# Performance work log

Hardware: AMD Instinct MI355X
Metric: run time of the kernel (lower is better)

Reference implementation:

```python
import jax, jax.numpy as jnp
import numpy as np

BN_EPS = 1e-5


def _bn(y, g, b, m, v):
    # BatchNorm1d in eval mode (running stats), faithful to torch's affine BN
    return (y - m) * jax.lax.rsqrt(v + BN_EPS) * g + b


def setup_inputs() -> dict:
    key = jax.random.key(0)
    ks = jax.random.split(key, 6)
    N, E, C_IN, C_OUT = 20000, 640000, 128, 256
    x = jax.random.normal(ks[0], (N, C_IN), dtype=jnp.float32)
    tpl_edge_index = jax.random.randint(ks[1], (2, E), 0, N, dtype=jnp.int64)
    def lin(k, o, i):
        return jax.random.normal(k, (o, i), dtype=jnp.float32) * 0.05
    inp = {
        'x': x,
        'tpl_edge_index': tpl_edge_index,
        'W1': lin(ks[2], C_OUT, 2 * C_IN), 'b1': jnp.zeros((C_OUT,), jnp.float32),
        'g1': jnp.ones((C_OUT,), jnp.float32), 'be1': jnp.zeros((C_OUT,), jnp.float32),
        'm1': jnp.zeros((C_OUT,), jnp.float32), 'v1': jnp.ones((C_OUT,), jnp.float32),
        'W2': lin(ks[3], C_OUT, C_OUT), 'b2': jnp.zeros((C_OUT,), jnp.float32),
        'g2': jnp.ones((C_OUT,), jnp.float32), 'be2': jnp.zeros((C_OUT,), jnp.float32),
        'm2': jnp.zeros((C_OUT,), jnp.float32), 'v2': jnp.ones((C_OUT,), jnp.float32),
        'W3': lin(ks[4], C_OUT, C_OUT), 'b3': jnp.zeros((C_OUT,), jnp.float32),
        'g3': jnp.ones((C_OUT,), jnp.float32), 'be3': jnp.zeros((C_OUT,), jnp.float32),
        'm3': jnp.zeros((C_OUT,), jnp.float32), 'v3': jnp.ones((C_OUT,), jnp.float32),
    }
    return inp


def reference(x, tpl_edge_index, W1, b1, g1, be1, m1, v1,
              W2, b2, g2, be2, m2, v2, W3, b3, g3, be3, m3, v3):
    N = x.shape[0]
    # remove_self_loops + add_self_loops: under max aggregation, duplicate
    # self-loop messages (x_j - x_i == 0) are idempotent, so appending one
    # self-loop per node is mathematically identical.
    loops = jnp.arange(N, dtype=tpl_edge_index.dtype)
    src = jnp.concatenate([tpl_edge_index[0], loops])  # x_j indices
    tgt = jnp.concatenate([tpl_edge_index[1], loops])  # x_i / aggregation indices
    x_i = x[tgt]                                       # [E+N, C_in]
    x_j = x[src]
    h = jnp.concatenate([x_i, x_j - x_i], axis=1)      # [E+N, 2*C_in]
    h = _bn(jax.nn.relu(h @ W1.T + b1), g1, be1, m1, v1)
    h = _bn(jax.nn.relu(h @ W2.T + b2), g2, be2, m2, v2)
    agg = jax.ops.segment_max(h, tgt, num_segments=N)  # scatter-max -> [N, C_out]
    out = _bn(jax.nn.relu(agg @ W3.T + b3), g3, be3, m3, v3)
    return out
```

## Files before the change

kernel.cpp:

```cpp
#include <hip/hip_runtime.h>
#include <stdint.h>

#define BN_EPS 1e-5f

typedef __bf16 bf16x8 __attribute__((ext_vector_type(8)));
typedef float  f32x4  __attribute__((ext_vector_type(4)));

__device__ __forceinline__ unsigned short f2bf(float f) {
    unsigned u = __float_as_uint(f);
    unsigned r = (u + 0x7FFFu + ((u >> 16) & 1u)) >> 16;
    return (unsigned short)r;
}
__device__ __forceinline__ unsigned pk2(float a, float b) {
    return (unsigned)f2bf(a) | ((unsigned)f2bf(b) << 16);
}
__device__ __forceinline__ unsigned ar2(unsigned p, unsigned q) {
    float pl = __uint_as_float(p << 16), ql = __uint_as_float(q << 16);
    float ph = __uint_as_float(p & 0xFFFF0000u), qh = __uint_as_float(q & 0xFFFF0000u);
    return pk2(fmaxf(pl + ql, 0.f), fmaxf(ph + qh, 0.f));
}
__device__ __forceinline__ unsigned short bfkey(unsigned short h) {
    return (h & 0x8000u) ? (unsigned short)(~h) : (unsigned short)(h | 0x8000u);
}
__device__ __forceinline__ unsigned short unbfkey(unsigned short k) {
    return (k & 0x8000u) ? (unsigned short)(k & 0x7FFFu) : (unsigned short)(~k);
}
__device__ __forceinline__ unsigned unb2(unsigned k0, unsigned k1) {
    return (unsigned)unbfkey((unsigned short)k0)
         | ((unsigned)unbfkey((unsigned short)k1) << 16);
}
__device__ __forceinline__ unsigned kk2(float a, float b) {
    return (unsigned)bfkey(f2bf(a)) | ((unsigned)bfkey(f2bf(b)) << 16);
}
__device__ __forceinline__ int swz(int row, int k) {
    const int blk = k >> 3;
    const int sb = (blk & 24) | ((blk ^ row) & 7);
    return (row << 8) + (sb << 3) + (k & 7);
}
__device__ __forceinline__ int swz128(int row, int k) {
    const int blk = k >> 3;
    const int sb = (blk & 8) | ((blk ^ row) & 7);
    return (row << 7) + (sb << 3) + (k & 7);
}

__global__ void prep_kernel(
    const float* __restrict__ x, const int* __restrict__ eidx,
    int E, int M, int NX,
    const float* __restrict__ W1, const float* __restrict__ W2, const float* __restrict__ W3,
    const float* __restrict__ b1, const float* __restrict__ g1, const float* __restrict__ be1,
    const float* __restrict__ m1, const float* __restrict__ v1,
    const float* __restrict__ b2, const float* __restrict__ g2, const float* __restrict__ be2,
    const float* __restrict__ m2, const float* __restrict__ v2,
    const float* __restrict__ b3, const float* __restrict__ g3, const float* __restrict__ be3,
    const float* __restrict__ m3, const float* __restrict__ v3,
    unsigned short* __restrict__ W1b, unsigned short* __restrict__ W2b,
    unsigned short* __restrict__ W3b, float* __restrict__ consts,
    unsigned short* __restrict__ xb, unsigned* __restrict__ count)
{
    const int idx = blockIdx.x * 256 + threadIdx.x;
    if (idx < 65536) {
        const int row = idx >> 8, c = idx & 255;
        float w1v = (c < 128) ? (W1[row * 256 + c] - W1[row * 256 + c + 128])
                              : W1[row * 256 + c];
        W1b[idx] = f2bf(w1v);
        const float s1c = g1[c] * rsqrtf(v1[c] + BN_EPS);
        W2b[idx] = f2bf(W2[idx] * s1c);
        W3b[idx] = f2bf(W3[idx]);
    }
    if (idx < 768) {
        const int l = idx >> 8, c = idx & 255;
        const float* bp  = l == 0 ? b1  : (l == 1 ? b2  : b3);
        const float* gp  = l == 0 ? g1  : (l == 1 ? g2  : g3);
        const float* bep = l == 0 ? be1 : (l == 1 ? be2 : be3);
        const float* mp  = l == 0 ? m1  : (l == 1 ? m2  : m3);
        const float* vp  = l == 0 ? v1  : (l == 1 ? v2  : v3);
        const float s = gp[c] * rsqrtf(vp[c] + BN_EPS);
        float bias = bp[c];
        if (l == 1) {
            float acc = 0.f;
            for (int k = 0; k < 256; k++) {
                const float s1k = g1[k] * rsqrtf(v1[k] + BN_EPS);
                acc += W2[c * 256 + k] * (be1[k] - m1[k] * s1k);
            }
            bias += acc;
        }
        consts[l * 768 + c]       = bias;
        consts[l * 768 + 256 + c] = s;
        consts[l * 768 + 512 + c] = bep[c] - mp[c] * s;
    }
    if (idx < NX) xb[idx] = f2bf(x[idx]);
    if (idx < M) {
        const int tgt = (idx < E) ? eidx[E + idx] : (idx - E);
        atomicAdd(&count[tgt], 1u);
    }
}

__global__ __launch_bounds__(512) void pq_kernel(
    const unsigned short* __restrict__ xb, int N,
    const unsigned short* __restrict__ W1b,
    const float* __restrict__ consts,
    unsigned short* __restrict__ Pb, unsigned short* __restrict__ Qb)
{
    __shared__ unsigned short Xs[64 * 128];

    const int t = threadIdx.x;
    const int base = blockIdx.x * 64;

    {
        const int row = t >> 3, part = t & 7;
        const int node = base + row;
        const int c0 = part * 16;
        if (node < N) {
            const unsigned short* s = xb + (size_t)node * 128 + c0;
            *(uint4*)&Xs[swz128(row, c0)]     = *(const uint4*)(s);
            *(uint4*)&Xs[swz128(row, c0 + 8)] = *(const uint4*)(s + 8);
        } else {
            const uint4 z = {0u, 0u, 0u, 0u};
            *(uint4*)&Xs[swz128(row, c0)]     = z;
            *(uint4*)&Xs[swz128(row, c0 + 8)] = z;
        }
    }
    __syncthreads();

    const int lane = t & 63;
    const int wv   = t >> 6;
    const int n16  = lane & 15;
    const int qd   = lane >> 4;
    const int wc   = wv * 32;

    const f32x4 vzero = {0.f, 0.f, 0.f, 0.f};

    #pragma unroll
    for (int ph = 0; ph < 2; ph++) {
        f32x4 acc[2][4];
        #pragma unroll
        for (int i = 0; i < 2; i++)
            #pragma unroll
            for (int j = 0; j < 4; j++) acc[i][j] = vzero;

        #pragma unroll
        for (int ks = 0; ks < 4; ks++) {
            const int k0 = ks * 32 + qd * 8;
            bf16x8 a[2], b[4];
            #pragma unroll
            for (int ci = 0; ci < 2; ci++)
                a[ci] = *(const bf16x8*)&W1b[(size_t)(wc + ci * 16 + n16) * 256 + ph * 128 + k0];
            #pragma unroll
            for (int rj = 0; rj < 4; rj++)
                b[rj] = *(const bf16x8*)&Xs[swz128(rj * 16 + n16, k0)];
            #pragma unroll
            for (int ci = 0; ci < 2; ci++)
                #pragma unroll
                for (int rj = 0; rj < 4; rj++)
                    acc[ci][rj] = __builtin_amdgcn_mfma_f32_16x16x32_bf16(a[ci], b[rj], acc[ci][rj], 0, 0, 0);
        }

        unsigned short* dst = ph == 0 ? Pb : Qb;
        #pragma unroll
        for (int ci = 0; ci < 2; ci++) {
            const int col0 = wc + ci * 16 + qd * 4;
            float4 bb = {0.f, 0.f, 0.f, 0.f};
            if (ph == 0) bb = *(const float4*)&consts[col0];
            #pragma unroll
            for (int rj = 0; rj < 4; rj++) {
                const int node = base + rj * 16 + n16;
                if (node < N) {
                    uint2 p = {pk2(acc[ci][rj][0] + bb.x, acc[ci][rj][1] + bb.y),
                               pk2(acc[ci][rj][2] + bb.z, acc[ci][rj][3] + bb.w)};
                    *(uint2*)(dst + (size_t)node * 256 + col0) = p;
                }
            }
        }
    }
}

__global__ __launch_bounds__(1024) void scan_kernel(
    const unsigned* __restrict__ count, unsigned* __restrict__ cursor, int N)
{
    __shared__ unsigned part[1024];
    const int t = threadIdx.x;
    const int per = (N + 1023) / 1024;
    const int b = t * per;
    unsigned s = 0;
    for (int i = 0; i < per; i++) if (b + i < N) s += count[b + i];
    part[t] = s;
    __syncthreads();
    for (int off = 1; off < 1024; off <<= 1) {
        unsigned v = (t >= off) ? part[t - off] : 0u;
        __syncthreads();
        part[t] += v;
        __syncthreads();
    }
    unsigned run = (t > 0) ? part[t - 1] : 0u;
    for (int i = 0; i < per; i++) {
        if (b + i < N) {
            unsigned c = count[b + i];
            cursor[b + i] = run;
            run += c;
        }
    }
}

__global__ void scatter_kernel(const int* __restrict__ eidx, int E, int M,
                               unsigned* __restrict__ cursor, int* __restrict__ spair)
{
    const int i = blockIdx.x * 256 + threadIdx.x;
    if (i < M) {
        int s, tg;
        if (i < E) { s = eidx[i]; tg = eidx[E + i]; }
        else       { s = tg = i - E; }
        const unsigned pos = atomicAdd(&cursor[tg], 1u);
        int2* p = (int2*)spair;
        p[pos] = make_int2(s, tg);
    }
}

__global__ __launch_bounds__(512) void msg_kernel(
    const unsigned short* __restrict__ Pb,
    const unsigned short* __restrict__ Qb,
    const int* __restrict__ spair,
    int M,
    const unsigned short* __restrict__ W2b,
    const float* __restrict__ consts,
    unsigned* __restrict__ agg)
{
    __shared__ unsigned short At[64 * 256];
    __shared__ int tgt_l[64];

    const int t = threadIdx.x;
    const int base = blockIdx.x * 64;

    {
        const int row = t >> 3, part = t & 7;
        const int slot = base + row;
        const int c0 = part * 32;
        if (slot < M) {
            const int2 pr = *(const int2*)(spair + 2 * slot);
            if (part == 0) tgt_l[row] = pr.y;
            const unsigned short* Pp = Pb + (size_t)pr.y * 256 + c0;
            const unsigned short* Qp = Qb + (size_t)pr.x * 256 + c0;
            uint4 P4[4], Q4[4];
            #pragma unroll
            for (int w = 0; w < 4; w++) P4[w] = *(const uint4*)(Pp + w * 8);
            #pragma unroll
            for (int w = 0; w < 4; w++) Q4[w] = *(const uint4*)(Qp + w * 8);
            #pragma unroll
            for (int w = 0; w < 4; w++) {
                uint4 u;
                u.x = ar2(P4[w].x, Q4[w].x);
                u.y = ar2(P4[w].y, Q4[w].y);
                u.z = ar2(P4[w].z, Q4[w].z);
                u.w = ar2(P4[w].w, Q4[w].w);
                *(uint4*)&At[swz(row, c0 + w * 8)] = u;
            }
        } else {
            if (part == 0) tgt_l[row] = -1;
            const uint4 z = {0u, 0u, 0u, 0u};
            #pragma unroll
            for (int w = 0; w < 4; w++) *(uint4*)&At[swz(row, c0 + w * 8)] = z;
        }
    }
    __syncthreads();

    const int lane = t & 63;
    const int wv   = t >> 6;
    const int n16  = lane & 15;
    const int qd   = lane >> 4;
    const int wc   = wv * 32;

    const f32x4 vzero = {0.f, 0.f, 0.f, 0.f};
    f32x4 acc[2][4];
    #pragma unroll
    for (int i = 0; i < 2; i++)
        #pragma unroll
        for (int j = 0; j < 4; j++) acc[i][j] = vzero;

    #pragma unroll
    for (int ks = 0; ks < 8; ks++) {
        const int k0 = ks * 32 + qd * 8;
        bf16x8 a[2], b[4];
        #pragma unroll
        for (int ci = 0; ci < 2; ci++)
            a[ci] = *(const bf16x8*)&W2b[(size_t)(wc + ci * 16 + n16) * 256 + k0];
        #pragma unroll
        for (int rj = 0; rj < 4; rj++)
            b[rj] = *(const bf16x8*)&At[swz(rj * 16 + n16, k0)];
        #pragma unroll
        for (int ci = 0; ci < 2; ci++)
            #pragma unroll
            for (int rj = 0; rj < 4; rj++)
                acc[ci][rj] = __builtin_amdgcn_mfma_f32_16x16x32_bf16(a[ci], b[rj], acc[ci][rj], 0, 0, 0);
    }
    __syncthreads();

    {
        const float* B2 = consts + 768;
        const float* S2 = consts + 768 + 256;
        const float* T2 = consts + 768 + 512;
        #pragma unroll
        for (int ci = 0; ci < 2; ci++) {
            const int col0 = wc + ci * 16 + qd * 4;
            const float4 bb = *(const float4*)&B2[col0];
            const float4 ss = *(const float4*)&S2[col0];
            const float4 tt = *(const float4*)&T2[col0];
            #pragma unroll
            for (int rj = 0; rj < 4; rj++) {
                const int row = rj * 16 + n16;
                float v0 = fmaxf(acc[ci][rj][0] + bb.x, 0.f) * ss.x + tt.x;
                float v1 = fmaxf(acc[ci][rj][1] + bb.y, 0.f) * ss.y + tt.y;
                float v2 = fmaxf(acc[ci][rj][2] + bb.z, 0.f) * ss.z + tt.z;
                float v3 = fmaxf(acc[ci][rj][3] + bb.w, 0.f) * ss.w + tt.w;
                uint2 p = {kk2(v0, v1), kk2(v2, v3)};
                *(uint2*)&At[swz(row, col0)] = p;
            }
        }
    }
    __syncthreads();

    {
        const int r0 = (wv & 3) * 16;
        const int cb = (wv >> 2) * 128 + lane * 2;
        const int myt = (lane < 16) ? tgt_l[r0 + lane] : -1;
        int curT = -1;
        unsigned m0 = 0, m1 = 0;
        for (int r = 0; r < 16; r++) {
            const int tg = __shfl(myt, r);
            const unsigned k2 = *(const unsigned*)&At[swz(r0 + r, cb)];
            const unsigned k0 = k2 & 0xFFFFu, k1 = k2 >> 16;
            if (tg != curT) {
                if (curT >= 0) {
                    unsigned* p = &agg[(size_t)curT * 256 + cb];
                    atomicMax(p, m0); atomicMax(p + 1, m1);
                }
                curT = tg; m0 = k0; m1 = k1;
            } else {
                m0 = m0 > k0 ? m0 : k0;
                m1 = m1 > k1 ? m1 : k1;
            }
        }
        if (curT >= 0) {
            unsigned* p = &agg[(size_t)curT * 256 + cb];
            atomicMax(p, m0); atomicMax(p + 1, m1);
        }
    }
}

__global__ __launch_bounds__(256) void out_kernel(
    const unsigned* __restrict__ agg, int N,
    const unsigned short* __restrict__ W3b,
    const float* __restrict__ consts,
    float* __restrict__ out)
{
    __shared__ unsigned short At[32 * 256];

    const int t = threadIdx.x;
    const int base = blockIdx.x * 32;

    {
        const int row = t >> 3, part = t & 7;
        const int node = base + row;
        const int c0 = part * 32;
        if (node < N) {
            const unsigned* ap = agg + (size_t)node * 256 + c0;
            #pragma unroll
            for (int w = 0; w < 4; w++) {
                uint4 a = *(const uint4*)(ap + w * 8);
                uint4 b = *(const uint4*)(ap + w * 8 + 4);
                uint4 p;
                p.x = unb2(a.x, a.y); p.y = unb2(a.z, a.w);
                p.z = unb2(b.x, b.y); p.w = unb2(b.z, b.w);
                *(uint4*)&At[swz(row, c0 + w * 8)] = p;
            }
        } else {
            const uint4 z = {0u, 0u, 0u, 0u};
            #pragma unroll
            for (int w = 0; w < 4; w++) *(uint4*)&At[swz(row, c0 + w * 8)] = z;
        }
    }
    __syncthreads();

    const int lane = t & 63;
    const int wv   = t >> 6;
    const int n16  = lane & 15;
    const int qd   = lane >> 4;
    const int wc   = wv * 64;

    const f32x4 vzero = {0.f, 0.f, 0.f, 0.f};
    f32x4 acc[2][4];
    #pragma unroll
    for (int i = 0; i < 2; i++)
        #pragma unroll
        for (int j = 0; j < 4; j++) acc[i][j] = vzero;

    #pragma unroll
    for (int ks = 0; ks < 8; ks++) {
        const int k0 = ks * 32 + qd * 8;
        bf16x8 a[2];
        #pragma unroll
        for (int ri = 0; ri < 2; ri++)
            a[ri] = *(const bf16x8*)&At[swz(ri * 16 + n16, k0)];
        #pragma unroll
        for (int ci = 0; ci < 4; ci++) {
            bf16x8 b = *(const bf16x8*)&W3b[(size_t)(wc + ci * 16 + n16) * 256 + k0];
            #pragma unroll
            for (int ri = 0; ri < 2; ri++)
                acc[ri][ci] = __builtin_amdgcn_mfma_f32_16x16x32_bf16(a[ri], b, acc[ri][ci], 0, 0, 0);
        }
    }

    {
        const float* B3 = consts + 1536;
        const float* S3 = consts + 1536 + 256;
        const float* T3 = consts + 1536 + 512;
        #pragma unroll
        for (int ci = 0; ci < 4; ci++) {
            const int col = wc + ci * 16 + n16;
            const float bb = B3[col], ss = S3[col], tt = T3[col];
            #pragma unroll
            for (int ri = 0; ri < 2; ri++) {
                #pragma unroll
                for (int r = 0; r < 4; r++) {
                    const int row = ri * 16 + qd * 4 + r;
                    const int node = base + row;
                    if (node < N) {
                        float v = fmaxf(acc[ri][ci][r] + bb, 0.f) * ss + tt;
                        out[(size_t)node * 256 + col] = v;
                    }
                }
            }
        }
    }
}

extern "C" void kernel_launch(void* const* d_in, const int* in_sizes, int n_in,
                              void* d_out, int out_size, void* d_ws, size_t ws_size,
                              hipStream_t stream)
{
    const float* x  = (const float*)d_in[0];
    const int* eidx = (const int*)d_in[1];
    const int N = in_sizes[0] / 128;
    const int NX = in_sizes[0];
    const int E = in_sizes[1] / 2;
    const int M = E + N;

    char* ws = (char*)d_ws;
    unsigned short* W1b = (unsigned short*)(ws);
    unsigned short* W2b = (unsigned short*)(ws + 131072);
    unsigned short* W3b = (unsigned short*)(ws + 262144);
    float* consts       = (float*)(ws + 393216);
    size_t off = 402432;
    unsigned short* xb  = (unsigned short*)(ws + off); off += (size_t)NX * 2;
    unsigned* agg       = (unsigned*)(ws + off);       off += (size_t)N * 256 * 4;
    unsigned* count     = (unsigned*)(ws + off);       off += (size_t)N * 4;
    unsigned* cursor    = (unsigned*)(ws + off);       off += (size_t)N * 4;
    int* spair          = (int*)(ws + off);            off += (size_t)M * 8;
    unsigned short* Pb  = (unsigned short*)(ws + off); off += (size_t)N * 256 * 2;
    unsigned short* Qb  = (unsigned short*)(ws + off);

    hipMemsetAsync(agg, 0, (size_t)N * 256 * 4, stream);
    hipMemsetAsync(count, 0, (size_t)N * 4, stream);

    int work = NX;
    if (M > work) work = M;
    if (65536 > work) work = 65536;
    hipLaunchKernelGGL(prep_kernel, dim3((work + 255) / 256), dim3(256), 0, stream,
        x, eidx, E, M, NX,
        (const float*)d_in[2], (const float*)d_in[8], (const float*)d_in[14],
        (const float*)d_in[3], (const float*)d_in[4], (const float*)d_in[5],
        (const float*)d_in[6], (const float*)d_in[7],
        (const float*)d_in[9], (const float*)d_in[10], (const float*)d_in[11],
        (const float*)d_in[12], (const float*)d_in[13],
        (const float*)d_in[15], (const float*)d_in[16], (const float*)d_in[17],
        (const float*)d_in[18], (const float*)d_in[19],
        W1b, W2b, W3b, consts, xb, count);

    hipLaunchKernelGGL(pq_kernel, dim3((N + 63) / 64), dim3(512), 0, stream,
        xb, N, W1b, consts, Pb, Qb);

    hipLaunchKernelGGL(scan_kernel, dim3(1), dim3(1024), 0, stream,
        count, cursor, N);
    hipLaunchKernelGGL(scatter_kernel, dim3((M + 255) / 256), dim3(256), 0, stream,
        eidx, E, M, cursor, spair);

    hipLaunchKernelGGL(msg_kernel, dim3((M + 63) / 64), dim3(512), 0, stream,
        Pb, Qb, spair, M, W2b, consts, agg);

    hipLaunchKernelGGL(out_kernel, dim3((N + 31) / 32), dim3(256), 0, stream,
        agg, N, W3b, consts, (float*)d_out);
}
```

Baseline: 517.3 us.

## Fold layer-2 BatchNorm into W3 and use sign-mask max keys

The layer-2 BN scale and shift are folded into W3 and the layer-3 bias, so msg_kernel only does bias+ReLU before aggregation. For channels with a negative BN scale, the ReLU output's bf16 bits are XOR-flipped, so max over the flipped value matches max over the scaled value. The per-channel masks are undone in out_kernel. Conversions now use hardware vector bf16 conversion instead of manual rounding. This cuts per-element ALU work in the message epilogue, but it assumes the existing max-aggregation scheme orders these flipped bit patterns correctly.

```diff
diff --git a/kernel.cpp b/kernel.cpp
--- a/kernel.cpp
+++ b/kernel.cpp
@@ -4,33 +4,28 @@
 #define BN_EPS 1e-5f
 
 typedef __bf16 bf16x8 __attribute__((ext_vector_type(8)));
+typedef __bf16 bf16x2 __attribute__((ext_vector_type(2)));
 typedef float  f32x4  __attribute__((ext_vector_type(4)));
+typedef float  f32x2  __attribute__((ext_vector_type(2)));
 
 __device__ __forceinline__ unsigned short f2bf(float f) {
     unsigned u = __float_as_uint(f);
     unsigned r = (u + 0x7FFFu + ((u >> 16) & 1u)) >> 16;
     return (unsigned short)r;
 }
-__device__ __forceinline__ unsigned pk2(float a, float b) {
-    return (unsigned)f2bf(a) | ((unsigned)f2bf(b) << 16);
+__device__ __forceinline__ unsigned pkb(float a, float b) {
+    f32x2 f; f.x = a; f.y = b;
+    bf16x2 h = __builtin_convertvector(f, bf16x2);
+    return *(unsigned*)&h;
 }
 __device__ __forceinline__ unsigned ar2(unsigned p, unsigned q) {
-    float pl = __uint_as_float(p << 16), ql = __uint_as_float(q << 16);
-    float ph = __uint_as_float(p & 0xFFFF0000u), qh = __uint_as_float(q & 0xFFFF0000u);
-    return pk2(fmaxf(pl + ql, 0.f), fmaxf(ph + qh, 0.f));
-}
-__device__ __forceinline__ unsigned short bfkey(unsigned short h) {
-    return (h & 0x8000u) ? (unsigned short)(~h) : (unsigned short)(h | 0x8000u);
-}
-__device__ __forceinline__ unsigned short unbfkey(unsigned short k) {
-    return (k & 0x8000u) ? (unsigned short)(k & 0x7FFFu) : (unsigned short)(~k);
-}
-__device__ __forceinline__ unsigned unb2(unsigned k0, unsigned k1) {
-    return (unsigned)unbfkey((unsigned short)k0)
-         | ((unsigned)unbfkey((unsigned short)k1) << 16);
-}
-__device__ __forceinline__ unsigned kk2(float a, float b) {
-    return (unsigned)bfkey(f2bf(a)) | ((unsigned)bfkey(f2bf(b)) << 16);
+    f32x2 a, b;
+    a.x = __uint_as_float(p << 16);
+    a.y = __uint_as_float(p & 0xFFFF0000u);
+    b.x = __uint_as_float(q << 16);
+    b.y = __uint_as_float(q & 0xFFFF0000u);
+    f32x2 s = a + b;
+    return pkb(fmaxf(s.x, 0.f), fmaxf(s.y, 0.f));
 }
 __device__ __forceinline__ int swz(int row, int k) {
     const int blk = k >> 3;
@@ -55,6 +50,7 @@
     const float* __restrict__ m3, const float* __restrict__ v3,
     unsigned short* __restrict__ W1b, unsigned short* __restrict__ W2b,
     unsigned short* __restrict__ W3b, float* __restrict__ consts,
+    unsigned* __restrict__ mask2,
     unsigned short* __restrict__ xb, unsigned* __restrict__ count)
 {
     const int idx = blockIdx.x * 256 + threadIdx.x;
@@ -65,7 +61,13 @@
         W1b[idx] = f2bf(w1v);
         const float s1c = g1[c] * rsqrtf(v1[c] + BN_EPS);
         W2b[idx] = f2bf(W2[idx] * s1c);
-        W3b[idx] = f2bf(W3[idx]);
+        const float s2c = g2[c] * rsqrtf(v2[c] + BN_EPS);
+        W3b[idx] = f2bf(W3[idx] * s2c);
+    }
+    if (idx < 128) {
+        const float sa = g2[2 * idx]     * rsqrtf(v2[2 * idx]     + BN_EPS);
+        const float sb = g2[2 * idx + 1] * rsqrtf(v2[2 * idx + 1] + BN_EPS);
+        mask2[idx] = (sa < 0.f ? 0xFFFFu : 0u) | ((sb < 0.f ? 0xFFFFu : 0u) << 16);
     }
     if (idx < 768) {
         const int l = idx >> 8, c = idx & 255;
@@ -83,6 +85,13 @@
                 acc += W2[c * 256 + k] * (be1[k] - m1[k] * s1k);
             }
             bias += acc;
+        } else if (l == 2) {
+            float acc = 0.f;
+            for (int k = 0; k < 256; k++) {
+                const float s2k = g2[k] * rsqrtf(v2[k] + BN_EPS);
+                acc += W3[c * 256 + k] * (be2[k] - m2[k] * s2k);
+            }
+            bias += acc;
         }
         consts[l * 768 + c]       = bias;
         consts[l * 768 + 256 + c] = s;
@@ -165,8 +174,8 @@
             for (int rj = 0; rj < 4; rj++) {
                 const int node = base + rj * 16 + n16;
                 if (node < N) {
-                    uint2 p = {pk2(acc[ci][rj][0] + bb.x, acc[ci][rj][1] + bb.y),
-                               pk2(acc[ci][rj][2] + bb.z, acc[ci][rj][3] + bb.w)};
+                    uint2 p = {pkb(acc[ci][rj][0] + bb.x, acc[ci][rj][1] + bb.y),
+                               pkb(acc[ci][rj][2] + bb.z, acc[ci][rj][3] + bb.w)};
                     *(uint2*)(dst + (size_t)node * 256 + col0) = p;
                 }
             }
@@ -222,6 +231,7 @@
     int M,
     const unsigned short* __restrict__ W2b,
     const float* __restrict__ consts,
+    const unsigned* __restrict__ mask2,
     unsigned* __restrict__ agg)
 {
     __shared__ unsigned short At[64 * 256];
@@ -295,22 +305,19 @@
 
     {
         const float* B2 = consts + 768;
-        const float* S2 = consts + 768 + 256;
-        const float* T2 = consts + 768 + 512;
         #pragma unroll
         for (int ci = 0; ci < 2; ci++) {
             const int col0 = wc + ci * 16 + qd * 4;
             const float4 bb = *(const float4*)&B2[col0];
-            const float4 ss = *(const float4*)&S2[col0];
-            const float4 tt = *(const float4*)&T2[col0];
+            const uint2 mk = *(const uint2*)&mask2[col0 >> 1];
             #pragma unroll
             for (int rj = 0; rj < 4; rj++) {
                 const int row = rj * 16 + n16;
-                float v0 = fmaxf(acc[ci][rj][0] + bb.x, 0.f) * ss.x + tt.x;
-                float v1 = fmaxf(acc[ci][rj][1] + bb.y, 0.f) * ss.y + tt.y;
-                float v2 = fmaxf(acc[ci][rj][2] + bb.z, 0.f) * ss.z + tt.z;
-                float v3 = fmaxf(acc[ci][rj][3] + bb.w, 0.f) * ss.w + tt.w;
-                uint2 p = {kk2(v0, v1), kk2(v2, v3)};
+                float r0 = fmaxf(acc[ci][rj][0] + bb.x, 0.f);
+                float r1 = fmaxf(acc[ci][rj][1] + bb.y, 0.f);
+                float r2 = fmaxf(acc[ci][rj][2] + bb.z, 0.f);
+                float r3 = fmaxf(acc[ci][rj][3] + bb.w, 0.f);
+                uint2 p = {pkb(r0, r1) ^ mk.x, pkb(r2, r3) ^ mk.y};
                 *(uint2*)&At[swz(row, col0)] = p;
             }
         }
@@ -349,6 +356,7 @@
     const unsigned* __restrict__ agg, int N,
     const unsigned short* __restrict__ W3b,
     const float* __restrict__ consts,
+    const unsigned* __restrict__ mask2,
     float* __restrict__ out)
 {
     __shared__ unsigned short At[32 * 256];
@@ -366,9 +374,12 @@
             for (int w = 0; w < 4; w++) {
                 uint4 a = *(const uint4*)(ap + w * 8);
                 uint4 b = *(const uint4*)(ap + w * 8 + 4);
+                const uint4 mk = *(const uint4*)&mask2[(c0 + w * 8) >> 1];
                 uint4 p;
-                p.x = unb2(a.x, a.y); p.y = unb2(a.z, a.w);
-                p.z = unb2(b.x, b.y); p.w = unb2(b.z, b.w);
+                p.x = (a.x | (a.y << 16)) ^ mk.x;
+                p.y = (a.z | (a.w << 16)) ^ mk.y;
+                p.z = (b.x | (b.y << 16)) ^ mk.z;
+                p.w = (b.z | (b.w << 16)) ^ mk.w;
                 *(uint4*)&At[swz(row, c0 + w * 8)] = p;
             }
         } else {
@@ -448,7 +459,8 @@
     unsigned short* W2b = (unsigned short*)(ws + 131072);
     unsigned short* W3b = (unsigned short*)(ws + 262144);
     float* consts       = (float*)(ws + 393216);
-    size_t off = 402432;
+    unsigned* mask2     = (unsigned*)(ws + 402432);
+    size_t off = 402944;
     unsigned short* xb  = (unsigned short*)(ws + off); off += (size_t)NX * 2;
     unsigned* agg       = (unsigned*)(ws + off);       off += (size_t)N * 256 * 4;
     unsigned* count     = (unsigned*)(ws + off);       off += (size_t)N * 4;
@@ -472,7 +484,7 @@
         (const float*)d_in[12], (const float*)d_in[13],
         (const float*)d_in[15], (const float*)d_in[16], (const float*)d_in[17],
         (const float*)d_in[18], (const float*)d_in[19],
-        W1b, W2b, W3b, consts, xb, count);
+        W1b, W2b, W3b, consts, mask2, xb, count);
 
     hipLaunchKernelGGL(pq_kernel, dim3((N + 63) / 64), dim3(512), 0, stream,
         xb, N, W1b, consts, Pb, Qb);
@@ -483,8 +495,8 @@
         eidx, E, M, cursor, spair);
 
     hipLaunchKernelGGL(msg_kernel, dim3((M + 63) / 64), dim3(512), 0, stream,
-        Pb, Qb, spair, M, W2b, consts, agg);
+        Pb, Qb, spair, M, W2b, consts, mask2, agg);
 
     hipLaunchKernelGGL(out_kernel, dim3((N + 31) / 32), dim3(256), 0, stream,
-        agg, N, W3b, consts, (float*)d_out);
-}
+        agg, N, W3b, consts, mask2, (float*)d_out);
+}
```

Result: faster. 490.9 us (-5.1%).
